# Optimization experiments

Hardware: AMD Instinct MI355X
Metric: run time of the kernel (lower is better)

## Reference

```python
import jax, jax.numpy as jnp
import numpy as np

SCALE = 100.0  # sharp-softmax temperature from the torch module

def _build_tables():
    # ByteToNibbleFFN: W1 is identity(256) so it is mathematically a no-op; keep W2.
    W2_b2n = np.zeros((256, 32), np.float32)
    bb = np.arange(256)
    W2_b2n[bb, bb >> 4] = 1.0
    W2_b2n[bb, 16 + (bb & 15)] = 1.0
    # NibbleAddWithCarryFFN tables
    W1_add = np.zeros((34, 512), np.float32)
    W2_sum = np.zeros((512, 16), np.float32)
    W2_cout = np.zeros((512, 2), np.float32)
    for a in range(16):
        for b in range(16):
            for c in range(2):
                idx = a * 32 + b * 2 + c
                W1_add[a, idx] = 1.0
                W1_add[16 + b, idx] = 1.0
                W1_add[32 + c, idx] = 1.0
                t = a + b + c
                W2_sum[idx, t & 15] = 1.0
                W2_cout[idx, 1 if t > 15 else 0] = 1.0
    # NibbleToByteFFN tables
    W1_n2b = np.zeros((32, 256), np.float32)
    W2_n2b = np.zeros((256, 256), np.float32)
    for h in range(16):
        for l in range(16):
            addr = h * 16 + l
            W1_n2b[h, addr] = 1.0
            W1_n2b[16 + l, addr] = 1.0
            W2_n2b[addr, (h << 4) | l] = 1.0
    return tuple(jnp.asarray(t) for t in (W2_b2n, W1_add, W2_sum, W2_cout, W1_n2b, W2_n2b))

W2_B2N, W1_ADD, W2_SUM, W2_COUT, W1_N2B, W2_N2B = _build_tables()

def _b2n(x):
    # byte [.,256] -> (high [.,16], low [.,16]); W1=eye(256) omitted (identity)
    out = x @ W2_B2N
    return out[..., :16], out[..., 16:]

def _nib_add(a, b, cin):
    combined = jnp.concatenate([a, b, cin], axis=-1)           # [.,34]
    address = jax.nn.softmax(combined @ W1_ADD * SCALE, axis=-1)  # [.,512]
    return address @ W2_SUM, address @ W2_COUT

def _n2b(high, low):
    combined = jnp.concatenate([high, low], axis=-1)           # [.,32]
    address = jax.nn.softmax(combined @ W1_N2B * SCALE, axis=-1)  # [.,256]
    return address @ W2_N2B

def setup_inputs() -> dict:
    key = jax.random.key(0)
    k1, k2 = jax.random.split(key)
    B = 32768
    a = jax.random.uniform(k1, (B, 4, 256), dtype=jnp.float32)
    b = jax.random.uniform(k2, (B, 4, 256), dtype=jnp.float32)
    return {"a": a, "b": b}

def reference(a, b):
    # NeuralALU.add: ripple-carry add over 4 bytes, 2 nibble adds per byte
    B = a.shape[0]
    carry = jnp.zeros((B, 2), a.dtype).at[:, 0].set(1.0)  # carry_zero one-hot
    out_bytes = []
    for i in range(4):  # fixed structural loop over bytes (carry dependence)
        ah, al = _b2n(a[:, i])
        bh, bl = _b2n(b[:, i])
        sl, carry = _nib_add(al, bl, carry)
        sh, carry = _nib_add(ah, bh, carry)
        out_bytes.append(_n2b(sh, sl))
    return jnp.stack(out_bytes, axis=1)  # [B,4,256]
```

## Files before the change

kernel.cpp:

```cpp
#include <hip/hip_runtime.h>

#define NIB_SCALE 100.0f

template<int CTRL>
__device__ __forceinline__ float fdpp(float x) {
    return __int_as_float(__builtin_amdgcn_update_dpp(
        0, __float_as_int(x), CTRL, 0xF, 0xF, true));
}

__device__ __forceinline__ float rsum16d(float v) {
    v += fdpp<0x121>(v);
    v += fdpp<0x122>(v);
    v += fdpp<0x124>(v);
    v += fdpp<0x128>(v);
    return v;
}
__device__ __forceinline__ float rmax16d(float v) {
    v = fmaxf(v, fdpp<0x121>(v));
    v = fmaxf(v, fdpp<0x122>(v));
    v = fmaxf(v, fdpp<0x124>(v));
    v = fmaxf(v, fdpp<0x128>(v));
    return v;
}
__device__ __forceinline__ float scan16d(float v) {
    v += fdpp<0x111>(v);
    v += fdpp<0x112>(v);
    v += fdpp<0x114>(v);
    v += fdpp<0x118>(v);
    return v;
}

__device__ __forceinline__ float softmax16d(float v) {
    float m = rmax16d(v);
    float e = expf(NIB_SCALE * (v - m));
    float s = rsum16d(e);
    return e / s;
}

#define GATHER_ROT(dst, src)            \
    dst[0]  = (src);                    \
    dst[1]  = fdpp<0x121>(src);         \
    dst[2]  = fdpp<0x122>(src);         \
    dst[3]  = fdpp<0x123>(src);         \
    dst[4]  = fdpp<0x124>(src);         \
    dst[5]  = fdpp<0x125>(src);         \
    dst[6]  = fdpp<0x126>(src);         \
    dst[7]  = fdpp<0x127>(src);         \
    dst[8]  = fdpp<0x128>(src);         \
    dst[9]  = fdpp<0x129>(src);         \
    dst[10] = fdpp<0x12A>(src);         \
    dst[11] = fdpp<0x12B>(src);         \
    dst[12] = fdpp<0x12C>(src);         \
    dst[13] = fdpp<0x12D>(src);         \
    dst[14] = fdpp<0x12E>(src);         \
    dst[15] = fdpp<0x12F>(src);

__global__ __launch_bounds__(256) void nalu_kernel(const float* __restrict__ A,
                                                   const float* __restrict__ B,
                                                   float* __restrict__ O,
                                                   int nrows) {
    __shared__ __align__(16) float sQL[16][16];
    __shared__ __align__(16) float sQH[16][16];
    __shared__ __align__(16) float sPSL[16][16];

    const int tid = threadIdx.x;
    const int k = tid & 15;
    const int g = tid >> 4;
    const int row = blockIdx.x * 16 + g;
    if (row >= nrows) return;
    const long base = (long)row * 1024;

    float pc0 = 1.0f, pc1 = 0.0f;

    #pragma unroll
    for (int byte = 0; byte < 4; ++byte) {
        const float* pa = A + base + byte * 256;
        const float* pb = B + base + byte * 256;

        float sa[16], sb[16];
        #pragma unroll
        for (int e = 0; e < 16; ++e) sa[e] = pa[16 * e + k];
        #pragma unroll
        for (int e = 0; e < 16; ++e) sb[e] = pb[16 * e + k];
        const float4* pa4 = (const float4*)(pa + 16 * k);
        const float4* pb4 = (const float4*)(pb + 16 * k);
        float4 ra0 = pa4[0], ra1 = pa4[1], ra2 = pa4[2], ra3 = pa4[3];
        float4 rb0 = pb4[0], rb1 = pb4[1], rb2 = pb4[2], rb3 = pb4[3];

        float al = 0.f, bl = 0.f;
        #pragma unroll
        for (int e = 0; e < 16; ++e) al += sa[e];
        #pragma unroll
        for (int e = 0; e < 16; ++e) bl += sb[e];
        float4 rat = make_float4(ra0.x + ra1.x + ra2.x + ra3.x,
                                 ra0.y + ra1.y + ra2.y + ra3.y,
                                 ra0.z + ra1.z + ra2.z + ra3.z,
                                 ra0.w + ra1.w + ra2.w + ra3.w);
        float4 rbt = make_float4(rb0.x + rb1.x + rb2.x + rb3.x,
                                 rb0.y + rb1.y + rb2.y + rb3.y,
                                 rb0.z + rb1.z + rb2.z + rb3.z,
                                 rb0.w + rb1.w + rb2.w + rb3.w);
        float ah = (rat.x + rat.y) + (rat.z + rat.w);
        float bh = (rbt.x + rbt.y) + (rbt.z + rbt.w);

        float pal = softmax16d(al);
        float pbl = softmax16d(bl);
        float pah = softmax16d(ah);
        float pbh = softmax16d(bh);

        sQL[g][k] = pbl;
        sQH[g][k] = pbh;

        float mirl = fdpp<0x140>(pbl);
        float mirh = fdpp<0x140>(pbh);
        float T15l = scan16d(mirl);
        float T15h = scan16d(mirh);
        float ov15l = rsum16d(pal * T15l);
        float c15l  = rsum16d(pal * mirl);
        float ov15h = rsum16d(pah * T15h);
        float c15h  = rsum16d(pah * mirh);
        float ov16l = ov15l - c15l;
        float ov16h = ov15h - c15h;

        float QL[16], QH[16];
        *(float4*)&QL[0]  = *(const float4*)&sQL[g][0];
        *(float4*)&QL[4]  = *(const float4*)&sQL[g][4];
        *(float4*)&QL[8]  = *(const float4*)&sQL[g][8];
        *(float4*)&QL[12] = *(const float4*)&sQL[g][12];
        *(float4*)&QH[0]  = *(const float4*)&sQH[g][0];
        *(float4*)&QH[4]  = *(const float4*)&sQH[g][4];
        *(float4*)&QH[8]  = *(const float4*)&sQH[g][8];
        *(float4*)&QH[12] = *(const float4*)&sQH[g][12];

        float GL[16], GH[16];
        GATHER_ROT(GL, pal)
        GATHER_ROT(GH, pah)
        float rl = 0.f, rh = 0.f;
        #pragma unroll
        for (int j = 0; j < 16; ++j) {
            rl = fmaf(GL[j], QL[j], rl);
            rh = fmaf(GH[j], QH[j], rh);
        }

        float rlm1  = fdpp<0x121>(rl);
        float slow  = pc0 * rl + pc1 * rlm1;
        float coutl = pc0 * ov16l + pc1 * ov15l;
        float qc1 = 1.0f / (1.0f + expf(NIB_SCALE * (1.0f - 2.0f * coutl)));
        float qc0 = 1.0f - qc1;

        float rhm1  = fdpp<0x121>(rh);
        float shigh = qc0 * rh + qc1 * rhm1;
        float couth = qc0 * ov16h + qc1 * ov15h;
        pc1 = 1.0f / (1.0f + expf(NIB_SCALE * (1.0f - 2.0f * couth)));
        pc0 = 1.0f - pc1;

        float psl = softmax16d(slow);
        float psh = softmax16d(shigh);

        sPSL[g][k] = psl;
        float PSL[16];
        *(float4*)&PSL[0]  = *(const float4*)&sPSL[g][0];
        *(float4*)&PSL[4]  = *(const float4*)&sPSL[g][4];
        *(float4*)&PSL[8]  = *(const float4*)&sPSL[g][8];
        *(float4*)&PSL[12] = *(const float4*)&sPSL[g][12];

        float* po = O + base + byte * 256 + 16 * k;
        #pragma unroll
        for (int c = 0; c < 4; ++c) {
            float4 o4 = make_float4(psh * PSL[4 * c + 0], psh * PSL[4 * c + 1],
                                    psh * PSL[4 * c + 2], psh * PSL[4 * c + 3]);
            *(float4*)(po + 4 * c) = o4;
        }
    }
}

extern "C" void kernel_launch(void* const* d_in, const int* in_sizes, int n_in,
                              void* d_out, int out_size, void* d_ws, size_t ws_size,
                              hipStream_t stream) {
    const float* A = (const float*)d_in[0];
    const float* B = (const float*)d_in[1];
    float* O = (float*)d_out;
    int nrows = in_sizes[0] / 1024;
    int grid = (nrows + 15) / 16;
    nalu_kernel<<<grid, 256, 0, stream>>>(A, B, O, nrows);
}
```

Baseline: 332.9 us.

## Parallelize bytes across 16-lane groups and resolve carry chain via shared scalars

Each 16-lane group now handles one byte of a row instead of looping serially over four bytes, so a block covers 4 rows and the grid grows fourfold. The byte-independent softmax and convolution work runs in parallel. The carry-dependent overflow scalars go to shared memory, where every group recomputes the short sigmoid carry chain. The change also switches to fast __expf and rewrites output stores so each lane writes contiguous float4s. It relies on wave64 lockstep for the shared-memory handoffs without an explicit barrier, and __expf may lose accuracy at the sharp scale.

New measurement: 303.8 us. -8.8%, faster.

```diff
diff --git a/kernel.cpp b/kernel.cpp
--- a/kernel.cpp
+++ b/kernel.cpp
@@ -9,32 +9,26 @@
 }
 
 __device__ __forceinline__ float rsum16d(float v) {
-    v += fdpp<0x121>(v);
-    v += fdpp<0x122>(v);
-    v += fdpp<0x124>(v);
-    v += fdpp<0x128>(v);
+    v += fdpp<0x121>(v); v += fdpp<0x122>(v); v += fdpp<0x124>(v); v += fdpp<0x128>(v);
     return v;
 }
 __device__ __forceinline__ float rmax16d(float v) {
-    v = fmaxf(v, fdpp<0x121>(v));
-    v = fmaxf(v, fdpp<0x122>(v));
-    v = fmaxf(v, fdpp<0x124>(v));
-    v = fmaxf(v, fdpp<0x128>(v));
+    v = fmaxf(v, fdpp<0x121>(v)); v = fmaxf(v, fdpp<0x122>(v));
+    v = fmaxf(v, fdpp<0x124>(v)); v = fmaxf(v, fdpp<0x128>(v));
     return v;
 }
 __device__ __forceinline__ float scan16d(float v) {
-    v += fdpp<0x111>(v);
-    v += fdpp<0x112>(v);
-    v += fdpp<0x114>(v);
-    v += fdpp<0x118>(v);
+    v += fdpp<0x111>(v); v += fdpp<0x112>(v); v += fdpp<0x114>(v); v += fdpp<0x118>(v);
     return v;
 }
-
 __device__ __forceinline__ float softmax16d(float v) {
     float m = rmax16d(v);
-    float e = expf(NIB_SCALE * (v - m));
+    float e = __expf(NIB_SCALE * (v - m));
     float s = rsum16d(e);
     return e / s;
+}
+__device__ __forceinline__ float sharp_sigmoid(float c) {
+    return 1.0f / (1.0f + __expf(NIB_SCALE * (1.0f - 2.0f * c)));
 }
 
 #define GATHER_ROT(dst, src)            \
@@ -62,115 +56,125 @@
     __shared__ __align__(16) float sQL[16][16];
     __shared__ __align__(16) float sQH[16][16];
     __shared__ __align__(16) float sPSL[16][16];
+    __shared__ __align__(16) float sPSH[16][16];
+    __shared__ __align__(16) float sOV[4][4][4];
 
     const int tid = threadIdx.x;
     const int k = tid & 15;
     const int g = tid >> 4;
-    const int row = blockIdx.x * 16 + g;
+    const int b = g & 3;
+    const int w = tid >> 6;
+    const int row = blockIdx.x * 4 + w;
     if (row >= nrows) return;
-    const long base = (long)row * 1024;
+    const long base = (long)row * 1024 + b * 256;
 
-    float pc0 = 1.0f, pc1 = 0.0f;
+    const float* pa = A + base;
+    const float* pb = B + base;
 
+    float a0 = 0, a1 = 0, a2 = 0, a3 = 0, b0 = 0, b1 = 0, b2 = 0, b3 = 0;
     #pragma unroll
-    for (int byte = 0; byte < 4; ++byte) {
-        const float* pa = A + base + byte * 256;
-        const float* pb = B + base + byte * 256;
+    for (int e = 0; e < 4; ++e) {
+        a0 += pa[16 * e + k];        b0 += pb[16 * e + k];
+        a1 += pa[16 * (e + 4) + k];  b1 += pb[16 * (e + 4) + k];
+        a2 += pa[16 * (e + 8) + k];  b2 += pb[16 * (e + 8) + k];
+        a3 += pa[16 * (e + 12) + k]; b3 += pb[16 * (e + 12) + k];
+    }
+    float al = (a0 + a1) + (a2 + a3);
+    float bl = (b0 + b1) + (b2 + b3);
+    const float4* pa4 = (const float4*)(pa + 16 * k);
+    const float4* pb4 = (const float4*)(pb + 16 * k);
+    float4 ra0 = pa4[0], ra1 = pa4[1], ra2 = pa4[2], ra3 = pa4[3];
+    float4 rb0 = pb4[0], rb1 = pb4[1], rb2 = pb4[2], rb3 = pb4[3];
+    float ah = ((ra0.x + ra0.y) + (ra0.z + ra0.w)) + ((ra1.x + ra1.y) + (ra1.z + ra1.w))
+             + ((ra2.x + ra2.y) + (ra2.z + ra2.w)) + ((ra3.x + ra3.y) + (ra3.z + ra3.w));
+    float bh = ((rb0.x + rb0.y) + (rb0.z + rb0.w)) + ((rb1.x + rb1.y) + (rb1.z + rb1.w))
+             + ((rb2.x + rb2.y) + (rb2.z + rb2.w)) + ((rb3.x + rb3.y) + (rb3.z + rb3.w));
 
-        float sa[16], sb[16];
-        #pragma unroll
-        for (int e = 0; e < 16; ++e) sa[e] = pa[16 * e + k];
-        #pragma unroll
-        for (int e = 0; e < 16; ++e) sb[e] = pb[16 * e + k];
-        const float4* pa4 = (const float4*)(pa + 16 * k);
-        const float4* pb4 = (const float4*)(pb + 16 * k);
-        float4 ra0 = pa4[0], ra1 = pa4[1], ra2 = pa4[2], ra3 = pa4[3];
-        float4 rb0 = pb4[0], rb1 = pb4[1], rb2 = pb4[2], rb3 = pb4[3];
+    float pal = softmax16d(al);
+    float pbl = softmax16d(bl);
+    float pah = softmax16d(ah);
+    float pbh = softmax16d(bh);
 
-        float al = 0.f, bl = 0.f;
-        #pragma unroll
-        for (int e = 0; e < 16; ++e) al += sa[e];
-        #pragma unroll
-        for (int e = 0; e < 16; ++e) bl += sb[e];
-        float4 rat = make_float4(ra0.x + ra1.x + ra2.x + ra3.x,
-                                 ra0.y + ra1.y + ra2.y + ra3.y,
-                                 ra0.z + ra1.z + ra2.z + ra3.z,
-                                 ra0.w + ra1.w + ra2.w + ra3.w);
-        float4 rbt = make_float4(rb0.x + rb1.x + rb2.x + rb3.x,
-                                 rb0.y + rb1.y + rb2.y + rb3.y,
-                                 rb0.z + rb1.z + rb2.z + rb3.z,
-                                 rb0.w + rb1.w + rb2.w + rb3.w);
-        float ah = (rat.x + rat.y) + (rat.z + rat.w);
-        float bh = (rbt.x + rbt.y) + (rbt.z + rbt.w);
+    sQL[g][k] = pbl;
+    sQH[g][k] = pbh;
 
-        float pal = softmax16d(al);
-        float pbl = softmax16d(bl);
-        float pah = softmax16d(ah);
-        float pbh = softmax16d(bh);
+    float mirl = fdpp<0x140>(pbl);
+    float mirh = fdpp<0x140>(pbh);
+    float T15l = scan16d(mirl);
+    float T15h = scan16d(mirh);
+    float ov15l = rsum16d(pal * T15l);
+    float c15l  = rsum16d(pal * mirl);
+    float ov15h = rsum16d(pah * T15h);
+    float c15h  = rsum16d(pah * mirh);
+    float ov16l = ov15l - c15l;
+    float ov16h = ov15h - c15h;
 
-        sQL[g][k] = pbl;
-        sQH[g][k] = pbh;
+    sOV[w][0][b] = ov16l;
+    sOV[w][1][b] = ov15l;
+    sOV[w][2][b] = ov16h;
+    sOV[w][3][b] = ov15h;
 
-        float mirl = fdpp<0x140>(pbl);
-        float mirh = fdpp<0x140>(pbh);
-        float T15l = scan16d(mirl);
-        float T15h = scan16d(mirh);
-        float ov15l = rsum16d(pal * T15l);
-        float c15l  = rsum16d(pal * mirl);
-        float ov15h = rsum16d(pah * T15h);
-        float c15h  = rsum16d(pah * mirh);
-        float ov16l = ov15l - c15l;
-        float ov16h = ov15h - c15h;
+    float QL[16], QH[16];
+    *(float4*)&QL[0]  = *(const float4*)&sQL[g][0];
+    *(float4*)&QL[4]  = *(const float4*)&sQL[g][4];
+    *(float4*)&QL[8]  = *(const float4*)&sQL[g][8];
+    *(float4*)&QL[12] = *(const float4*)&sQL[g][12];
+    float GL[16];
+    GATHER_ROT(GL, pal)
+    float rl = 0.f;
+    #pragma unroll
+    for (int j = 0; j < 16; ++j) rl = fmaf(GL[j], QL[j], rl);
 
-        float QL[16], QH[16];
-        *(float4*)&QL[0]  = *(const float4*)&sQL[g][0];
-        *(float4*)&QL[4]  = *(const float4*)&sQL[g][4];
-        *(float4*)&QL[8]  = *(const float4*)&sQL[g][8];
-        *(float4*)&QL[12] = *(const float4*)&sQL[g][12];
-        *(float4*)&QH[0]  = *(const float4*)&sQH[g][0];
-        *(float4*)&QH[4]  = *(const float4*)&sQH[g][4];
-        *(float4*)&QH[8]  = *(const float4*)&sQH[g][8];
-        *(float4*)&QH[12] = *(const float4*)&sQH[g][12];
+    *(float4*)&QH[0]  = *(const float4*)&sQH[g][0];
+    *(float4*)&QH[4]  = *(const float4*)&sQH[g][4];
+    *(float4*)&QH[8]  = *(const float4*)&sQH[g][8];
+    *(float4*)&QH[12] = *(const float4*)&sQH[g][12];
+    float GH[16];
+    GATHER_ROT(GH, pah)
+    float rh = 0.f;
+    #pragma unroll
+    for (int j = 0; j < 16; ++j) rh = fmaf(GH[j], QH[j], rh);
 
-        float GL[16], GH[16];
-        GATHER_ROT(GL, pal)
-        GATHER_ROT(GH, pah)
-        float rl = 0.f, rh = 0.f;
-        #pragma unroll
-        for (int j = 0; j < 16; ++j) {
-            rl = fmaf(GL[j], QL[j], rl);
-            rh = fmaf(GH[j], QH[j], rh);
-        }
+    float4 O16L = *(const float4*)&sOV[w][0][0];
+    float4 O15L = *(const float4*)&sOV[w][1][0];
+    float4 O16H = *(const float4*)&sOV[w][2][0];
+    float4 O15H = *(const float4*)&sOV[w][3][0];
 
-        float rlm1  = fdpp<0x121>(rl);
-        float slow  = pc0 * rl + pc1 * rlm1;
-        float coutl = pc0 * ov16l + pc1 * ov15l;
-        float qc1 = 1.0f / (1.0f + expf(NIB_SCALE * (1.0f - 2.0f * coutl)));
-        float qc0 = 1.0f - qc1;
+    float qc1_0 = sharp_sigmoid(O16L.x);
+    float qc0_0 = 1.f - qc1_0;
+    float pc1_1 = sharp_sigmoid(qc0_0 * O16H.x + qc1_0 * O15H.x);
+    float pc0_1 = 1.f - pc1_1;
+    float qc1_1 = sharp_sigmoid(pc0_1 * O16L.y + pc1_1 * O15L.y);
+    float qc0_1 = 1.f - qc1_1;
+    float pc1_2 = sharp_sigmoid(qc0_1 * O16H.y + qc1_1 * O15H.y);
+    float pc0_2 = 1.f - pc1_2;
+    float qc1_2 = sharp_sigmoid(pc0_2 * O16L.z + pc1_2 * O15L.z);
+    float qc0_2 = 1.f - qc1_2;
+    float pc1_3 = sharp_sigmoid(qc0_2 * O16H.z + qc1_2 * O15H.z);
+    float pc0_3 = 1.f - pc1_3;
+    float qc1_3 = sharp_sigmoid(pc0_3 * O16L.w + pc1_3 * O15L.w);
+    float qc0_3 = 1.f - qc1_3;
 
-        float rhm1  = fdpp<0x121>(rh);
-        float shigh = qc0 * rh + qc1 * rhm1;
-        float couth = qc0 * ov16h + qc1 * ov15h;
-        pc1 = 1.0f / (1.0f + expf(NIB_SCALE * (1.0f - 2.0f * couth)));
-        pc0 = 1.0f - pc1;
+    float pc0 = b == 0 ? 1.f   : b == 1 ? pc0_1 : b == 2 ? pc0_2 : pc0_3;
+    float pc1 = b == 0 ? 0.f   : b == 1 ? pc1_1 : b == 2 ? pc1_2 : pc1_3;
+    float qc0 = b == 0 ? qc0_0 : b == 1 ? qc0_1 : b == 2 ? qc0_2 : qc0_3;
+    float qc1 = b == 0 ? qc1_0 : b == 1 ? qc1_1 : b == 2 ? qc1_2 : qc1_3;
 
-        float psl = softmax16d(slow);
-        float psh = softmax16d(shigh);
+    float slow  = pc0 * rl + pc1 * fdpp<0x121>(rl);
+    float shigh = qc0 * rh + qc1 * fdpp<0x121>(rh);
 
-        sPSL[g][k] = psl;
-        float PSL[16];
-        *(float4*)&PSL[0]  = *(const float4*)&sPSL[g][0];
-        *(float4*)&PSL[4]  = *(const float4*)&sPSL[g][4];
-        *(float4*)&PSL[8]  = *(const float4*)&sPSL[g][8];
-        *(float4*)&PSL[12] = *(const float4*)&sPSL[g][12];
+    float psl = softmax16d(slow);
+    float psh = softmax16d(shigh);
+    sPSL[g][k] = psl;
+    sPSH[g][k] = psh;
 
-        float* po = O + base + byte * 256 + 16 * k;
-        #pragma unroll
-        for (int c = 0; c < 4; ++c) {
-            float4 o4 = make_float4(psh * PSL[4 * c + 0], psh * PSL[4 * c + 1],
-                                    psh * PSL[4 * c + 2], psh * PSL[4 * c + 3]);
-            *(float4*)(po + 4 * c) = o4;
-        }
+    float4 pslq = *(const float4*)&sPSL[g][4 * (k & 3)];
+    float* po = O + base;
+    #pragma unroll
+    for (int c = 0; c < 4; ++c) {
+        float hs = sPSH[g][4 * c + (k >> 2)];
+        float4 o4 = make_float4(hs * pslq.x, hs * pslq.y, hs * pslq.z, hs * pslq.w);
+        *(float4*)(po + 64 * c + 4 * k) = o4;
     }
 }
 
@@ -181,6 +185,6 @@
     const float* B = (const float*)d_in[1];
     float* O = (float*)d_out;
     int nrows = in_sizes[0] / 1024;
-    int grid = (nrows + 15) / 16;
+    int grid = (nrows + 3) / 4;
     nalu_kernel<<<grid, 256, 0, stream>>>(A, B, O, nrows);
 }
```
